# Kernel optimization log

Hardware: AMD Instinct MI355X
Metric: run time of the kernel (lower is better)

Reference implementation:

```python
import jax, jax.numpy as jnp
import numpy as np

OBJ_DIM, REL_DIM, EFF_DIM = 5, 1, 100
REL_HID, OBJ_HID, OUT_DIM = 150, 100, 2


def _init_linear(key, fan_in, fan_out):
    kw, kb = jax.random.split(key)
    bound = 1.0 / np.sqrt(fan_in)
    W = jax.random.uniform(kw, (fan_in, fan_out), jnp.float32, -bound, bound)
    b = jax.random.uniform(kb, (fan_out,), jnp.float32, -bound, bound)
    return W, b


def setup_inputs() -> dict:
    key = jax.random.key(0)
    ks = jax.random.split(key, 12)
    B, N, R = 64, 100, 9900
    inp = {
        "objects": jax.random.normal(ks[0], (B, N, OBJ_DIM), jnp.float32),
        "sender_relations": jax.random.uniform(ks[1], (B, N, R), jnp.float32),
        "receiver_relations": jax.random.uniform(ks[2], (B, N, R), jnp.float32),
        "relation_info": jax.random.normal(ks[3], (B, R, REL_DIM), jnp.float32),
    }
    # relational MLP: (2*obj + rel) -> 150 -> 150 -> effect_dim, ReLU after each
    rW1, rb1 = _init_linear(ks[4], 2 * OBJ_DIM + REL_DIM, REL_HID)
    rW2, rb2 = _init_linear(ks[5], REL_HID, REL_HID)
    rW3, rb3 = _init_linear(ks[6], REL_HID, EFF_DIM)
    # object MLP: (obj + effect) -> 100 -> 100 -> 2
    oW1, ob1 = _init_linear(ks[7], OBJ_DIM + EFF_DIM, OBJ_HID)
    oW2, ob2 = _init_linear(ks[8], OBJ_HID, OBJ_HID)
    oW3, ob3 = _init_linear(ks[9], OBJ_HID, OUT_DIM)
    inp.update(rW1=rW1, rb1=rb1, rW2=rW2, rb2=rb2, rW3=rW3, rb3=rb3,
               oW1=oW1, ob1=ob1, oW2=oW2, ob2=ob2, oW3=oW3, ob3=ob3)
    return inp


def _relational_mlp(x, rW1, rb1, rW2, rb2, rW3, rb3):
    h = jax.nn.relu(x @ rW1 + rb1)
    h = jax.nn.relu(h @ rW2 + rb2)
    return jax.nn.relu(h @ rW3 + rb3)


def _object_mlp(x, oW1, ob1, oW2, ob2, oW3, ob3):
    h = jax.nn.relu(x @ oW1 + ob1)
    h = jax.nn.relu(h @ oW2 + ob2)
    return h @ oW3 + ob3


def reference(objects, sender_relations, receiver_relations, relation_info,
              rW1, rb1, rW2, rb2, rW3, rb3, oW1, ob1, oW2, ob2, oW3, ob3):
    # gather: [B,R,N] @ [B,N,D] -> [B,R,D]
    senders = jnp.einsum('bnr,bnd->brd', sender_relations, objects)
    receivers = jnp.einsum('bnr,bnd->brd', receiver_relations, objects)
    rel_in = jnp.concatenate([senders, receivers, relation_info], axis=2)
    effects = _relational_mlp(rel_in, rW1, rb1, rW2, rb2, rW3, rb3)  # [B,R,E]
    # scatter: [B,N,R] @ [B,R,E] -> [B,N,E]
    effect_receivers = jnp.einsum('bnr,bre->bne', receiver_relations, effects)
    obj_in = jnp.concatenate([objects, effect_receivers], axis=2)
    return _object_mlp(obj_in, oW1, ob1, oW2, ob2, oW3, ob3)  # [B,N,2]
```

## Files before the change

### kernel.cpp

```cpp
#include <hip/hip_runtime.h>
#include <hip/hip_bf16.h>

#define B_    64
#define N_    100
#define R_    9900
#define OBJD  5
#define EFF   100

typedef __bf16 bf16x8 __attribute__((ext_vector_type(8)));
typedef __bf16 bf16x2 __attribute__((ext_vector_type(2)));
typedef short  short8v __attribute__((ext_vector_type(8)));
typedef float  f32x4  __attribute__((ext_vector_type(4)));

__device__ __forceinline__ ushort f2bf(float f) {
    __bf16 h = (__bf16)f;
    return __builtin_bit_cast(ushort, h);
}
__device__ __forceinline__ unsigned pk2(float a, float b) {
    bf16x2 v; v[0] = (__bf16)a; v[1] = (__bf16)b;
    return __builtin_bit_cast(unsigned, v);
}
__device__ __forceinline__ float bf2f(ushort u) {
    union { unsigned u; float f; } x; x.u = ((unsigned)u) << 16;
    return x.f;
}

#define WTR_OBJ 52096

__global__ __launch_bounds__(256) void k_prepw(
    const float* __restrict__ W1, const float* __restrict__ W2,
    const float* __restrict__ W3, const float* __restrict__ O1,
    const float* __restrict__ O2, const float* __restrict__ O3,
    ushort* __restrict__ WTR)
{
    const int img = blockIdx.x;
    if (img == 0) {
        for (int idx = threadIdx.x; idx < 6400; idx += 256) {
            const int c = idx / 40, k = idx - (idx/40)*40;
            WTR[idx] = f2bf((c < 150 && k < 11) ? W1[k*150 + c] : 0.f);
        }
    } else if (img == 1) {
        for (int idx = threadIdx.x; idx < 26880; idx += 256) {
            const int c = idx / 168, k = idx - (idx/168)*168;
            WTR[6400 + idx] = f2bf((c < 150 && k < 150) ? W2[k*150 + c] : 0.f);
        }
    } else if (img == 2) {
        for (int idx = threadIdx.x; idx < 18816; idx += 256) {
            const int c = idx / 168, k = idx - (idx/168)*168;
            WTR[33280 + idx] = f2bf((c < 100 && k < 150) ? W3[k*100 + c] : 0.f);
        }
    } else {
        const int j = img - 3;
        ushort* dst = WTR + WTR_OBJ + (size_t)j*11520;
        for (int idx = threadIdx.x; idx < 11520; idx += 256) {
            const int cc = idx / 72, kk = idx - (idx/72)*72;
            float v = 0.f;
            if (kk < 64) {
                if (j < 4) {
                    const int kg = j*64 + kk;
                    int row = -1;
                    if (kg < 5) row = kg;
                    else if (kg >= 8 && kg < 108) row = kg - 3;
                    else if (kg >= 108 && kg < 208) row = kg - 103;
                    if (cc < 100 && row >= 0) v = O1[row*100 + cc];
                } else if (j < 6) {
                    const int kg = (j-4)*64 + kk;
                    if (cc < 100 && kg < 100) v = O2[kg*100 + cc];
                } else {
                    const int kg = (j-6)*64 + kk;
                    if (cc < 2 && kg < 100) v = O3[kg*2 + cc];
                }
            }
            dst[idx] = f2bf(v);
        }
    }
}

#define LW1 0
#define LW2 6400
#define LW3 33280
#define LBA 52096
#define LBB 60160
#define LACT 68224
#define LBIAS 78976
#define LGB  79776
#define LTOT 81312

__global__ __launch_bounds__(512, 1) void k_relmlp_p(
    const float* __restrict__ obj, const float* __restrict__ SR,
    const float* __restrict__ RR, const float* __restrict__ RI,
    const ushort* __restrict__ WTR,
    const float* __restrict__ b1, const float* __restrict__ b2,
    const float* __restrict__ b3, float* __restrict__ ER)
{
    __shared__ __align__(16) ushort lds[LTOT];
    const int t  = threadIdx.x;
    const int b  = blockIdx.x >> 2;
    const int qt = blockIdx.x & 3;
    const int lane = t & 63, w = t >> 6;
    const int lo = lane & 15, hi = lane >> 4;
    const int mt = w & 3, nh = w >> 2;
    const int q  = t & 7,  rr = t >> 3;

    #pragma unroll
    for (int j = 0; j < 13; ++j) {
        const int idx = t + j*512;
        if (idx < 6512)
            reinterpret_cast<uint4*>(lds)[idx] =
                reinterpret_cast<const uint4*>(WTR)[idx];
    }
    {
        float* bias_w = (float*)(lds + LBIAS);
        if (t < 150)      bias_w[t] = b1[t];
        else if (t < 300) bias_w[t] = b2[t-150];
        else if (t < 400) bias_w[t] = b3[t-300];
    }
    if (t < 216) {
        ushort* base = lds + ((t < 108) ? LBA : LBB) + 100*72;
        const int k = (t < 108) ? t : t - 108;
        *reinterpret_cast<uint4*>(base + k*8) = make_uint4(0u, 0u, 0u, 0u);
    }
    if (t < 64) {
        ushort* gb0 = lds + LGB + t*24;
        gb0[11] = 0;
        *reinterpret_cast<ushort4*>(&gb0[12]) = make_ushort4(0,0,0,0);
        *reinterpret_cast<ushort4*>(&gb0[16]) = make_ushort4(0,0,0,0);
        *reinterpret_cast<ushort4*>(&gb0[20]) = make_ushort4(0,0,0,0);
    }

    float objv[13][5];
    {
        const int n0 = q*13;
        #pragma unroll
        for (int i = 0; i < 13; ++i) {
            const int n = n0 + i;
            #pragma unroll
            for (int d = 0; d < 5; ++d)
                objv[i][d] = (n < N_) ? obj[(size_t)b*500 + n*5 + d] : 0.f;
        }
    }

    const int tile0 = qt*39;
    const int tile1 = (tile0 + 39 < 155) ? tile0 + 39 : 155;

    ushort* bufA = lds + LBA;
    ushort* bufB = lds + LBB;
    ushort* act  = lds + LACT;
    ushort* gb   = lds + LGB;
    const float* bias = (const float*)(lds + LBIAS);

    f32x4 acc_er[7];
    #pragma unroll
    for (int ct = 0; ct < 7; ++ct) acc_er[ct] = (f32x4){0.f, 0.f, 0.f, 0.f};

    float4 psr[4], prr[4];
    float pri = 0.f, pri_n = 0.f;
    auto load4 = [&](float4* p, const float* M, int tile) {
        const int rr0 = tile*64;
        const int nr = (R_ - rr0 < 64) ? R_ - rr0 : 64;
        #pragma unroll
        for (int i = 0; i < 4; ++i) {
            const int idx = t + i*512;
            const int ci = idx < 1600 ? idx : 1599;
            const int n = ci >> 4, qq = ci & 15;
            const int col = (qq*4 < nr) ? qq*4 : 0;
            p[i] = *reinterpret_cast<const float4*>(
                &M[((size_t)b*N_ + n)*R_ + rr0 + col]);
        }
    };
    auto store4 = [&](const float4* p, ushort* dst, int nrow) {
        #pragma unroll
        for (int i = 0; i < 4; ++i) {
            const int idx = t + i*512;
            if (idx < 1600) {
                const int n = idx >> 4, qq = idx & 15;
                float4 v = p[i];
                if (qq*4 >= nrow) v = make_float4(0.f, 0.f, 0.f, 0.f);
                uint2 u; u.x = pk2(v.x, v.y); u.y = pk2(v.z, v.w);
                *reinterpret_cast<uint2*>(&dst[n*72 + qq*4]) = u;
            }
        }
    };
    auto loadRI = [&](int tile) -> float {
        const int rr0 = tile*64;
        return (t < 64 && rr0 + t < R_) ? RI[(size_t)b*R_ + rr0 + t] : 0.f;
    };

    load4(psr, SR, tile0);
    load4(prr, RR, tile0);
    pri = loadRI(tile0);
    __syncthreads();

    for (int tile = tile0; tile < tile1; ++tile) {
        const int r0 = tile*64;
        const int nrow = (R_ - r0 < 64) ? R_ - r0 : 64;

        store4(psr, bufA, nrow);
        store4(prr, bufB, nrow);
        if (tile + 1 < tile1) {
            load4(psr, SR, tile+1);
            load4(prr, RR, tile+1);
            pri_n = loadRI(tile+1);
        }
        __syncthreads();

        {
            float s0=0.f,s1=0.f,s2=0.f,s3=0.f,s4=0.f;
            float g0=0.f,g1=0.f,g2=0.f,g3=0.f,g4=0.f;
            const int n0 = q*13;
            #pragma unroll
            for (int i = 0; i < 13; ++i) {
                const int n = n0 + i;
                const float ms = bf2f(bufA[n*72 + rr]);
                const float mr = bf2f(bufB[n*72 + rr]);
                s0 += ms*objv[i][0]; s1 += ms*objv[i][1]; s2 += ms*objv[i][2];
                s3 += ms*objv[i][3]; s4 += ms*objv[i][4];
                g0 += mr*objv[i][0]; g1 += mr*objv[i][1]; g2 += mr*objv[i][2];
                g3 += mr*objv[i][3]; g4 += mr*objv[i][4];
            }
            #pragma unroll
            for (int msk = 1; msk < 8; msk <<= 1) {
                s0 += __shfl_xor(s0, msk); s1 += __shfl_xor(s1, msk);
                s2 += __shfl_xor(s2, msk); s3 += __shfl_xor(s3, msk);
                s4 += __shfl_xor(s4, msk);
                g0 += __shfl_xor(g0, msk); g1 += __shfl_xor(g1, msk);
                g2 += __shfl_xor(g2, msk); g3 += __shfl_xor(g3, msk);
                g4 += __shfl_xor(g4, msk);
            }
            if (q < 5) {
                const float sv = (q==0)?s0:(q==1)?s1:(q==2)?s2:(q==3)?s3:s4;
                const float gv = (q==0)?g0:(q==1)?g1:(q==2)?g2:(q==3)?g3:g4;
                gb[rr*24 + q]     = f2bf(sv);
                gb[rr*24 + 5 + q] = f2bf(gv);
            }
            if (t < 64) gb[t*24 + 10] = f2bf(pri);
            pri = pri_n;
        }
        __syncthreads();

        {
            f32x4 acc[5];
            #pragma unroll
            for (int j = 0; j < 5; ++j) {
                const int c = (nh*5 + j)*16 + lo;
                const float bv = (c < 150) ? bias[c] : 0.f;
                acc[j][0]=bv; acc[j][1]=bv; acc[j][2]=bv; acc[j][3]=bv;
            }
            bf16x8 a = __builtin_bit_cast(bf16x8, (short8v)0);
            if (hi < 2)
                a = *reinterpret_cast<const bf16x8*>(
                    &gb[(mt*16 + lo)*24 + hi*8]);
            #pragma unroll
            for (int j = 0; j < 5; ++j) {
                const int ct = nh*5 + j;
                const bf16x8 bb = *reinterpret_cast<const bf16x8*>(
                    &lds[LW1 + (ct*16 + lo)*40 + hi*8]);
                acc[j] = __builtin_amdgcn_mfma_f32_16x16x32_bf16(a, bb, acc[j], 0,0,0);
            }
            #pragma unroll
            for (int j = 0; j < 5; ++j) {
                const int ct = nh*5 + j;
                #pragma unroll
                for (int r = 0; r < 4; ++r)
                    act[(mt*16 + hi*4 + r)*168 + ct*16 + lo] =
                        f2bf(fmaxf(acc[j][r], 0.f));
            }
            __syncthreads();
        }
        {
            f32x4 acc[5];
            #pragma unroll
            for (int j = 0; j < 5; ++j) {
                const int c = (nh*5 + j)*16 + lo;
                const float bv = (c < 150) ? bias[150 + c] : 0.f;
                acc[j][0]=bv; acc[j][1]=bv; acc[j][2]=bv; acc[j][3]=bv;
            }
            #pragma unroll
            for (int ks = 0; ks < 5; ++ks) {
                const bf16x8 a = *reinterpret_cast<const bf16x8*>(
                    &act[(mt*16 + lo)*168 + ks*32 + hi*8]);
                #pragma unroll
                for (int j = 0; j < 5; ++j) {
                    const int ct = nh*5 + j;
                    const bf16x8 bb = *reinterpret_cast<const bf16x8*>(
                        &lds[LW2 + (ct*16 + lo)*168 + ks*32 + hi*8]);
                    acc[j] = __builtin_amdgcn_mfma_f32_16x16x32_bf16(a, bb, acc[j], 0,0,0);
                }
            }
            __syncthreads();
            #pragma unroll
            for (int j = 0; j < 5; ++j) {
                const int ct = nh*5 + j;
                #pragma unroll
                for (int r = 0; r < 4; ++r)
                    act[(mt*16 + hi*4 + r)*168 + ct*16 + lo] =
                        f2bf(fmaxf(acc[j][r], 0.f));
            }
            __syncthreads();
        }
        {
            const int nct = nh ? 3 : 4;
            f32x4 acc[4];
            #pragma unroll
            for (int j = 0; j < 4; ++j) {
                const int c = (nh*4 + j)*16 + lo;
                const float bv = (c < 100) ? bias[300 + c] : 0.f;
                acc[j][0]=bv; acc[j][1]=bv; acc[j][2]=bv; acc[j][3]=bv;
            }
            #pragma unroll
            for (int ks = 0; ks < 5; ++ks) {
                const bf16x8 a = *reinterpret_cast<const bf16x8*>(
                    &act[(mt*16 + lo)*168 + ks*32 + hi*8]);
                #pragma unroll
                for (int j = 0; j < 4; ++j) {
                    if (j < nct) {
                        const int ct = nh*4 + j;
                        const bf16x8 bb = *reinterpret_cast<const bf16x8*>(
                            &lds[LW3 + (ct*16 + lo)*168 + ks*32 + hi*8]);
                        acc[j] = __builtin_amdgcn_mfma_f32_16x16x32_bf16(a, bb, acc[j], 0,0,0);
                    }
                }
            }
            #pragma unroll
            for (int j = 0; j < 4; ++j) {
                if (j < nct) {
                    const int e = (nh*4 + j)*16 + lo;
                    if (e < 100) {
                        uint2 u;
                        u.x = pk2(fmaxf(acc[j][0], 0.f), fmaxf(acc[j][1], 0.f));
                        u.y = pk2(fmaxf(acc[j][2], 0.f), fmaxf(acc[j][3], 0.f));
                        *reinterpret_cast<uint2*>(&bufA[e*72 + mt*16 + hi*4]) = u;
                    }
                }
            }
            __syncthreads();
        }

        if (w < 7) {
            #pragma unroll
            for (int ks = 0; ks < 2; ++ks) {
                const bf16x8 a = *reinterpret_cast<const bf16x8*>(
                    &bufB[(w*16 + lo)*72 + ks*32 + hi*8]);
                #pragma unroll
                for (int ct = 0; ct < 7; ++ct) {
                    const bf16x8 bb = *reinterpret_cast<const bf16x8*>(
                        &bufA[(ct*16 + lo)*72 + ks*32 + hi*8]);
                    acc_er[ct] = __builtin_amdgcn_mfma_f32_16x16x32_bf16(
                        a, bb, acc_er[ct], 0, 0, 0);
                }
            }
        }
        __syncthreads();
    }

    if (w < 7) {
        float* ERq = ER + ((size_t)qt*B_ + b)*(size_t)(N_*EFF);
        #pragma unroll
        for (int ct = 0; ct < 7; ++ct) {
            const int e = ct*16 + lo;
            if (e < EFF) {
                #pragma unroll
                for (int rg = 0; rg < 4; ++rg) {
                    const int n = w*16 + hi*4 + rg;
                    if (n < N_)
                        ERq[n*EFF + e] = acc_er[ct][rg];
                }
            }
        }
    }
}

__device__ __forceinline__ void img_load(const ushort* __restrict__ g,
                                         uint4* pre, int t) {
    #pragma unroll
    for (int j = 0; j < 6; ++j) {
        int idx = t + j*256;
        int cidx = idx < 1440 ? idx : 1439;
        pre[j] = *reinterpret_cast<const uint4*>(g + (size_t)cidx*8);
    }
}
__device__ __forceinline__ void img_store(const uint4* pre, ushort* wt, int t) {
    #pragma unroll
    for (int j = 0; j < 6; ++j) {
        int idx = t + j*256;
        if (idx < 1440)
            *reinterpret_cast<uint4*>(wt + (size_t)idx*8) = pre[j];
    }
}

template<int COUT, int NCHUNK, int LASTKS, int NCT, bool RELU, int EPI, int ASTR>
__device__ __forceinline__ void mfma_layerO(
    const ushort* __restrict__ WT, const float* __restrict__ Bias,
    ushort* act, ushort* wt, int t, float* gout, int grow0)
{
    const int lane = t & 63;
    const int wv   = t >> 6;
    const int lo   = lane & 15;
    const int hi   = lane >> 4;

    f32x4 acc[2][NCT];
    #pragma unroll
    for (int ct = 0; ct < NCT; ++ct) {
        const int c = ct*16 + lo;
        const float bv = (c < COUT) ? Bias[c] : 0.f;
        #pragma unroll
        for (int m = 0; m < 2; ++m) {
            acc[m][ct][0] = bv; acc[m][ct][1] = bv;
            acc[m][ct][2] = bv; acc[m][ct][3] = bv;
        }
    }

    uint4 pre[6];
    img_load(WT, pre, t);
    #pragma unroll
    for (int q = 0; q < NCHUNK; ++q) {
        __syncthreads();
        img_store(pre, wt, t);
        if (q + 1 < NCHUNK) img_load(WT + (size_t)(q+1)*11520, pre, t);
        __syncthreads();
        const int nks = (q == NCHUNK-1) ? LASTKS : 2;
        #pragma unroll
        for (int ks = 0; ks < 2; ++ks) {
            if (ks < nks) {
                const int kg = q*64 + ks*32;
                const bf16x8 a0 = *reinterpret_cast<const bf16x8*>(
                    &act[(wv*32 +      lo)*ASTR + kg + hi*8]);
                const bf16x8 a1 = *reinterpret_cast<const bf16x8*>(
                    &act[(wv*32 + 16 + lo)*ASTR + kg + hi*8]);
                #pragma unroll
                for (int ct = 0; ct < NCT; ++ct) {
                    const bf16x8 b = *reinterpret_cast<const bf16x8*>(
                        &wt[(ct*16 + lo)*72 + ks*32 + hi*8]);
                    acc[0][ct] = __builtin_amdgcn_mfma_f32_16x16x32_bf16(
                        a0, b, acc[0][ct], 0, 0, 0);
                    acc[1][ct] = __builtin_amdgcn_mfma_f32_16x16x32_bf16(
                        a1, b, acc[1][ct], 0, 0, 0);
                }
            }
        }
    }

    __syncthreads();
    if (EPI == 0) {
        #pragma unroll
        for (int m = 0; m < 2; ++m)
            #pragma unroll
            for (int ct = 0; ct < NCT; ++ct)
                #pragma unroll
                for (int r = 0; r < 4; ++r) {
                    float v = acc[m][ct][r];
                    if (RELU) v = fmaxf(v, 0.f);
                    act[(wv*32 + m*16 + hi*4 + r)*ASTR + ct*16 + lo] = f2bf(v);
                }
    } else {
        #pragma unroll
        for (int m = 0; m < 2; ++m)
            #pragma unroll
            for (int r = 0; r < 4; ++r)
                if (lo < 2)
                    gout[(size_t)(grow0 + wv*32 + m*16 + hi*4 + r)*2 + lo] =
                        acc[m][0][r];
    }
    __syncthreads();
}

#define OSTR 232
#define ERSL ((size_t)B_*N_*EFF)

__global__ __launch_bounds__(256, 1) void k_objmlp_mfma(
    const float* __restrict__ obj, const float* __restrict__ ER,
    const ushort* __restrict__ WO,
    const float* __restrict__ ob1, const float* __restrict__ ob2,
    const float* __restrict__ ob3, float* __restrict__ out)
{
    __shared__ __align__(16) ushort act[128*OSTR];
    __shared__ __align__(16) ushort wt[160*72];
    const int t = threadIdx.x;
    const int rowbase = blockIdx.x * 128;

    float4 per[13];
    #pragma unroll
    for (int j = 0; j < 13; ++j) {
        const int idx = t + j*256;
        const int ci = idx < 3200 ? idx : 3199;
        const int row = ci / 25, c = ci - row*25;
        const float* p = &ER[(size_t)(rowbase + row)*100 + c*4];
        const float4 a0 = *reinterpret_cast<const float4*>(p);
        const float4 a1 = *reinterpret_cast<const float4*>(p + ERSL);
        const float4 a2 = *reinterpret_cast<const float4*>(p + 2*ERSL);
        const float4 a3 = *reinterpret_cast<const float4*>(p + 3*ERSL);
        per[j] = make_float4(a0.x + a1.x + a2.x + a3.x,
                             a0.y + a1.y + a2.y + a3.y,
                             a0.z + a1.z + a2.z + a3.z,
                             a0.w + a1.w + a2.w + a3.w);
    }
    #pragma unroll
    for (int j = 0; j < 13; ++j) {
        const int idx = t + j*256;
        if (idx < 3200) {
            const int row = idx / 25, c = idx - row*25;
            ushort h[4], l[4];
            #pragma unroll
            for (int k = 0; k < 4; ++k) {
                const float f = ((const float*)&per[j])[k];
                h[k] = f2bf(f);
                l[k] = f2bf(f - bf2f(h[k]));
            }
            *reinterpret_cast<ushort4*>(&act[row*OSTR + 8 + c*4]) =
                make_ushort4(h[0], h[1], h[2], h[3]);
            *reinterpret_cast<ushort4*>(&act[row*OSTR + 108 + c*4]) =
                make_ushort4(l[0], l[1], l[2], l[3]);
        }
    }
    #pragma unroll
    for (int j = 0; j < 3; ++j) {
        const int idx = t + j*256;
        if (idx < 640) {
            const int row = idx / 5, d = idx - row*5;
            act[row*OSTR + d] = f2bf(obj[(size_t)(rowbase + row)*5 + d]);
        }
    }
    #pragma unroll
    for (int j = 0; j < 2; ++j) {
        const int idx = t + j*256;
        if (idx < 384) {
            const int row = idx / 3, c = 5 + (idx - row*3);
            act[row*OSTR + c] = 0;
        }
    }
    #pragma unroll
    for (int j = 0; j < 2; ++j) {
        const int idx = t + j*256;
        if (idx < 512) {
            const int row = idx >> 2, p = idx & 3;
            *reinterpret_cast<ushort4*>(&act[row*OSTR + 208 + p*4]) =
                make_ushort4(0, 0, 0, 0);
        }
    }

    mfma_layerO<100, 4, 1, 7, true,  0, OSTR>(WO,           ob1, act, wt, t, nullptr, 0);
    mfma_layerO<100, 2, 2, 7, true,  0, OSTR>(WO + 4*11520, ob2, act, wt, t, nullptr, 0);
    mfma_layerO<2,   2, 2, 1, false, 2, OSTR>(WO + 6*11520, ob3, act, wt, t, out, rowbase);
}

extern "C" void kernel_launch(void* const* d_in, const int* in_sizes, int n_in,
                              void* d_out, int out_size, void* d_ws, size_t ws_size,
                              hipStream_t stream)
{
    const float* objects = (const float*)d_in[0];
    const float* SR      = (const float*)d_in[1];
    const float* RR      = (const float*)d_in[2];
    const float* RI      = (const float*)d_in[3];
    const float* rW1 = (const float*)d_in[4];  const float* rb1 = (const float*)d_in[5];
    const float* rW2 = (const float*)d_in[6];  const float* rb2 = (const float*)d_in[7];
    const float* rW3 = (const float*)d_in[8];  const float* rb3 = (const float*)d_in[9];
    const float* oW1 = (const float*)d_in[10]; const float* ob1 = (const float*)d_in[11];
    const float* oW2 = (const float*)d_in[12]; const float* ob2 = (const float*)d_in[13];
    const float* oW3 = (const float*)d_in[14]; const float* ob3 = (const float*)d_in[15];
    float* out = (float*)d_out;

    char* ws = (char*)d_ws;
    float*  ERp = (float*)ws;
    ushort* WTR = (ushort*)(ws + (size_t)4*B_*N_*EFF*sizeof(float));

    k_prepw<<<dim3(11), 256, 0, stream>>>(rW1, rW2, rW3, oW1, oW2, oW3, WTR);

    k_relmlp_p<<<dim3(256), 512, 0, stream>>>(objects, SR, RR, RI, WTR,
                                              rb1, rb2, rb3, ERp);

    k_objmlp_mfma<<<dim3(50), 256, 0, stream>>>(objects, ERp, WTR + WTR_OBJ,
                                                ob1, ob2, ob3, out);
}
```

Before: 366.9 us.

## Stage relation tiles via async global-to-LDS loads and hold W2 in registers

Replaces the register-prefetch-then-store staging of the sender/receiver relation tiles with direct global_load_lds transfers into fp32 LDS buffers. The next tile's transfer is issued after the gather phase so it overlaps the MLP compute. The layer-2 weight fragments are moved from LDS into registers, which frees LDS space, and launch bounds now ask for 2 blocks per CU. The costs are higher register pressure from the 25 bf16x8 weight fragments, an extra bf16 conversion pass for the receiver matrix, and possible register spills under the new occupancy target.

```diff
diff --git a/kernel.cpp b/kernel.cpp
--- a/kernel.cpp
+++ b/kernel.cpp
@@ -9,7 +9,6 @@
 
 typedef __bf16 bf16x8 __attribute__((ext_vector_type(8)));
 typedef __bf16 bf16x2 __attribute__((ext_vector_type(2)));
-typedef short  short8v __attribute__((ext_vector_type(8)));
 typedef float  f32x4  __attribute__((ext_vector_type(4)));
 
 __device__ __forceinline__ ushort f2bf(float f) {
@@ -23,6 +22,10 @@
 __device__ __forceinline__ float bf2f(ushort u) {
     union { unsigned u; float f; } x; x.u = ((unsigned)u) << 16;
     return x.f;
+}
+
+__device__ __forceinline__ void gload_lds16(const float* g, float* l) {
+    __builtin_amdgcn_global_load_lds((const void*)g, (void*)l, 16, 0, 0);
 }
 
 #define WTR_OBJ 52096
@@ -76,17 +79,18 @@
     }
 }
 
-#define LW1 0
-#define LW2 6400
-#define LW3 33280
-#define LBA 52096
-#define LBB 60160
-#define LACT 68224
-#define LBIAS 78976
-#define LGB  79776
-#define LTOT 81312
-
-__global__ __launch_bounds__(512, 1) void k_relmlp_p(
+#define LW1   0
+#define LW3   6400
+#define LSR32 25216
+#define LRR32 38528
+#define LRRNR 51840
+#define LEBUF 59904
+#define LACT  67968
+#define LBIAS 78720
+#define LGB   79520
+#define LTOT  81056
+
+__global__ __launch_bounds__(512, 2) void k_relmlp_p(
     const float* __restrict__ obj, const float* __restrict__ SR,
     const float* __restrict__ RR, const float* __restrict__ RI,
     const ushort* __restrict__ WTR,
@@ -102,12 +106,27 @@
     const int mt = w & 3, nh = w >> 2;
     const int q  = t & 7,  rr = t >> 3;
 
-    #pragma unroll
-    for (int j = 0; j < 13; ++j) {
+    float*  SRf  = (float*)(lds + LSR32);
+    float*  RRf  = (float*)(lds + LRR32);
+    ushort* RRnr = lds + LRRNR;
+    ushort* EB   = lds + LEBUF;
+    ushort* act  = lds + LACT;
+    ushort* gb   = lds + LGB;
+    const float* bias = (const float*)(lds + LBIAS);
+
+    #pragma unroll
+    for (int j = 0; j < 2; ++j) {
         const int idx = t + j*512;
-        if (idx < 6512)
+        if (idx < 800)
             reinterpret_cast<uint4*>(lds)[idx] =
                 reinterpret_cast<const uint4*>(WTR)[idx];
+    }
+    #pragma unroll
+    for (int j = 0; j < 5; ++j) {
+        const int idx = t + j*512;
+        if (idx < 2352)
+            reinterpret_cast<uint4*>(lds + LW3)[idx] =
+                reinterpret_cast<const uint4*>(WTR + 33280)[idx];
     }
     {
         float* bias_w = (float*)(lds + LBIAS);
@@ -115,13 +134,17 @@
         else if (t < 300) bias_w[t] = b2[t-150];
         else if (t < 400) bias_w[t] = b3[t-300];
     }
+    if (t < 256) {
+        SRf[6400 + t] = 0.f;
+        RRf[6400 + t] = 0.f;
+    }
     if (t < 216) {
-        ushort* base = lds + ((t < 108) ? LBA : LBB) + 100*72;
+        ushort* base = ((t < 108) ? RRnr : EB) + 100*72;
         const int k = (t < 108) ? t : t - 108;
         *reinterpret_cast<uint4*>(base + k*8) = make_uint4(0u, 0u, 0u, 0u);
     }
     if (t < 64) {
-        ushort* gb0 = lds + LGB + t*24;
+        ushort* gb0 = gb + t*24;
         gb0[11] = 0;
         *reinterpret_cast<ushort4*>(&gb0[12]) = make_ushort4(0,0,0,0);
         *reinterpret_cast<ushort4*>(&gb0[16]) = make_ushort4(0,0,0,0);
@@ -140,44 +163,35 @@
         }
     }
 
+    bf16x8 w2f[5][5];
+    #pragma unroll
+    for (int ks = 0; ks < 5; ++ks)
+        #pragma unroll
+        for (int j = 0; j < 5; ++j)
+            w2f[ks][j] = *reinterpret_cast<const bf16x8*>(
+                &WTR[6400 + ((nh*5 + j)*16 + lo)*168 + ks*32 + hi*8]);
+
     const int tile0 = qt*39;
     const int tile1 = (tile0 + 39 < 155) ? tile0 + 39 : 155;
 
-    ushort* bufA = lds + LBA;
-    ushort* bufB = lds + LBB;
-    ushort* act  = lds + LACT;
-    ushort* gb   = lds + LGB;
-    const float* bias = (const float*)(lds + LBIAS);
-
     f32x4 acc_er[7];
     #pragma unroll
     for (int ct = 0; ct < 7; ++ct) acc_er[ct] = (f32x4){0.f, 0.f, 0.f, 0.f};
 
-    float4 psr[4], prr[4];
-    float pri = 0.f, pri_n = 0.f;
-    auto load4 = [&](float4* p, const float* M, int tile) {
-        const int rr0 = tile*64;
-        const int nr = (R_ - rr0 < 64) ? R_ - rr0 : 64;
-        #pragma unroll
-        for (int i = 0; i < 4; ++i) {
-            const int idx = t + i*512;
-            const int ci = idx < 1600 ? idx : 1599;
-            const int n = ci >> 4, qq = ci & 15;
-            const int col = (qq*4 < nr) ? qq*4 : 0;
-            p[i] = *reinterpret_cast<const float4*>(
-                &M[((size_t)b*N_ + n)*R_ + rr0 + col]);
-        }
-    };
-    auto store4 = [&](const float4* p, ushort* dst, int nrow) {
-        #pragma unroll
-        for (int i = 0; i < 4; ++i) {
-            const int idx = t + i*512;
-            if (idx < 1600) {
-                const int n = idx >> 4, qq = idx & 15;
-                float4 v = p[i];
-                if (qq*4 >= nrow) v = make_float4(0.f, 0.f, 0.f, 0.f);
-                uint2 u; u.x = pk2(v.x, v.y); u.y = pk2(v.z, v.w);
-                *reinterpret_cast<uint2*>(&dst[n*72 + qq*4]) = u;
+    auto stage_async = [&](int tile) {
+        const int r0n = tile*64;
+        const int cb  = (lane & 15)*4;
+        const int cc  = (r0n + cb + 3 < R_) ? cb : 0;
+        const int rw  = lane >> 4;
+        const float* gS = SR + (size_t)b*N_*R_ + r0n + cc;
+        const float* gR = RR + (size_t)b*N_*R_ + r0n + cc;
+        #pragma unroll
+        for (int g0 = 0; g0 < 4; ++g0) {
+            const int g = w + g0*8;
+            if (g < 25) {
+                const int n = g*4;
+                gload_lds16(gS + (size_t)(n + rw)*R_, &SRf[n*64]);
+                gload_lds16(gR + (size_t)(n + rw)*R_, &RRf[n*64]);
             }
         }
     };
@@ -186,23 +200,15 @@
         return (t < 64 && rr0 + t < R_) ? RI[(size_t)b*R_ + rr0 + t] : 0.f;
     };
 
-    load4(psr, SR, tile0);
-    load4(prr, RR, tile0);
+    float pri, pri_n = 0.f;
+    stage_async(tile0);
     pri = loadRI(tile0);
+    asm volatile("s_waitcnt vmcnt(0)" ::: "memory");
     __syncthreads();
 
     for (int tile = tile0; tile < tile1; ++tile) {
         const int r0 = tile*64;
         const int nrow = (R_ - r0 < 64) ? R_ - r0 : 64;
-
-        store4(psr, bufA, nrow);
-        store4(prr, bufB, nrow);
-        if (tile + 1 < tile1) {
-            load4(psr, SR, tile+1);
-            load4(prr, RR, tile+1);
-            pri_n = loadRI(tile+1);
-        }
-        __syncthreads();
 
         {
             float s0=0.f,s1=0.f,s2=0.f,s3=0.f,s4=0.f;
@@ -211,8 +217,8 @@
             #pragma unroll
             for (int i = 0; i < 13; ++i) {
                 const int n = n0 + i;
-                const float ms = bf2f(bufA[n*72 + rr]);
-                const float mr = bf2f(bufB[n*72 + rr]);
+                const float ms = SRf[n*64 + rr];
+                const float mr = RRf[n*64 + rr];
                 s0 += ms*objv[i][0]; s1 += ms*objv[i][1]; s2 += ms*objv[i][2];
                 s3 += ms*objv[i][3]; s4 += ms*objv[i][4];
                 g0 += mr*objv[i][0]; g1 += mr*objv[i][1]; g2 += mr*objv[i][2];
@@ -234,9 +240,29 @@
                 gb[rr*24 + 5 + q] = f2bf(gv);
             }
             if (t < 64) gb[t*24 + 10] = f2bf(pri);
-            pri = pri_n;
+        }
+        {
+            #pragma unroll
+            for (int i = 0; i < 4; ++i) {
+                const int idx = t + i*512;
+                if (idx < 1600) {
+                    const int n = idx >> 4, qq = idx & 15;
+                    f32x4 v = *reinterpret_cast<const f32x4*>(&RRf[n*64 + qq*4]);
+                    if (qq*4 + 0 >= nrow) v[0] = 0.f;
+                    if (qq*4 + 1 >= nrow) v[1] = 0.f;
+                    if (qq*4 + 2 >= nrow) v[2] = 0.f;
+                    if (qq*4 + 3 >= nrow) v[3] = 0.f;
+                    uint2 u; u.x = pk2(v[0], v[1]); u.y = pk2(v[2], v[3]);
+                    *reinterpret_cast<uint2*>(&RRnr[n*72 + qq*4]) = u;
+                }
+            }
         }
         __syncthreads();
+
+        if (tile + 1 < tile1) {
+            stage_async(tile + 1);
+            pri_n = loadRI(tile + 1);
+        }
 
         {
             f32x4 acc[5];
@@ -246,7 +272,7 @@
                 const float bv = (c < 150) ? bias[c] : 0.f;
                 acc[j][0]=bv; acc[j][1]=bv; acc[j][2]=bv; acc[j][3]=bv;
             }
-            bf16x8 a = __builtin_bit_cast(bf16x8, (short8v)0);
+            bf16x8 a = {};
             if (hi < 2)
                 a = *reinterpret_cast<const bf16x8*>(
                     &gb[(mt*16 + lo)*24 + hi*8]);
@@ -280,12 +306,9 @@
                 const bf16x8 a = *reinterpret_cast<const bf16x8*>(
                     &act[(mt*16 + lo)*168 + ks*32 + hi*8]);
                 #pragma unroll
-                for (int j = 0; j < 5; ++j) {
-                    const int ct = nh*5 + j;
-                    const bf16x8 bb = *reinterpret_cast<const bf16x8*>(
-                        &lds[LW2 + (ct*16 + lo)*168 + ks*32 + hi*8]);
-                    acc[j] = __builtin_amdgcn_mfma_f32_16x16x32_bf16(a, bb, acc[j], 0,0,0);
-                }
+                for (int j = 0; j < 5; ++j)
+                    acc[j] = __builtin_amdgcn_mfma_f32_16x16x32_bf16(
+                        a, w2f[ks][j], acc[j], 0,0,0);
             }
             __syncthreads();
             #pragma unroll
@@ -329,7 +352,7 @@
                         uint2 u;
                         u.x = pk2(fmaxf(acc[j][0], 0.f), fmaxf(acc[j][1], 0.f));
                         u.y = pk2(fmaxf(acc[j][2], 0.f), fmaxf(acc[j][3], 0.f));
-                        *reinterpret_cast<uint2*>(&bufA[e*72 + mt*16 + hi*4]) = u;
+                        *reinterpret_cast<uint2*>(&EB[e*72 + mt*16 + hi*4]) = u;
                     }
                 }
             }
@@ -340,17 +363,19 @@
             #pragma unroll
             for (int ks = 0; ks < 2; ++ks) {
                 const bf16x8 a = *reinterpret_cast<const bf16x8*>(
-                    &bufB[(w*16 + lo)*72 + ks*32 + hi*8]);
+                    &RRnr[(w*16 + lo)*72 + ks*32 + hi*8]);
                 #pragma unroll
                 for (int ct = 0; ct < 7; ++ct) {
                     const bf16x8 bb = *reinterpret_cast<const bf16x8*>(
-                        &bufA[(ct*16 + lo)*72 + ks*32 + hi*8]);
+                        &EB[(ct*16 + lo)*72 + ks*32 + hi*8]);
                     acc_er[ct] = __builtin_amdgcn_mfma_f32_16x16x32_bf16(
                         a, bb, acc_er[ct], 0, 0, 0);
                 }
             }
         }
+        asm volatile("s_waitcnt vmcnt(0)" ::: "memory");
         __syncthreads();
+        pri = pri_n;
     }
 
     if (w < 7) {
```

New measurement: 627.8 us. +71.1%, slower.

## Hold part of W2 in registers to shrink LDS and fit two blocks per CU

Applied to the files above, without the earlier changes.

The first three k-slices of the layer-2 weight fragments move into per-thread registers, loaded once from global memory. Only the remaining two k-slices of W2 stay in LDS, in a compacted layout. The LDS footprint drops to about 132KB, and launch bounds change to allow two 512-thread blocks per CU, aiming to overlap memory streaming and MFMA work across blocks. The cost is 60 extra VGPRs per thread under a tighter register cap, which risks spills.

```diff
diff --git a/kernel.cpp b/kernel.cpp
--- a/kernel.cpp
+++ b/kernel.cpp
@@ -9,8 +9,8 @@
 
 typedef __bf16 bf16x8 __attribute__((ext_vector_type(8)));
 typedef __bf16 bf16x2 __attribute__((ext_vector_type(2)));
-typedef short  short8v __attribute__((ext_vector_type(8)));
 typedef float  f32x4  __attribute__((ext_vector_type(4)));
+typedef unsigned u32x4v __attribute__((ext_vector_type(4)));
 
 __device__ __forceinline__ ushort f2bf(float f) {
     __bf16 h = (__bf16)f;
@@ -76,17 +76,17 @@
     }
 }
 
-#define LW1 0
-#define LW2 6400
-#define LW3 33280
-#define LBA 52096
-#define LBB 60160
-#define LACT 68224
-#define LBIAS 78976
-#define LGB  79776
-#define LTOT 81312
-
-__global__ __launch_bounds__(512, 1) void k_relmlp_p(
+#define LW1   0
+#define LW3   6400
+#define LW2H  25216
+#define LBA   36736
+#define LBB   44800
+#define LACT  52864
+#define LBIAS 63616
+#define LGB   64416
+#define LTOT  65952
+
+__global__ __launch_bounds__(512, 2) void k_relmlp_p(
     const float* __restrict__ obj, const float* __restrict__ SR,
     const float* __restrict__ RR, const float* __restrict__ RI,
     const ushort* __restrict__ WTR,
@@ -102,12 +102,34 @@
     const int mt = w & 3, nh = w >> 2;
     const int q  = t & 7,  rr = t >> 3;
 
-    #pragma unroll
-    for (int j = 0; j < 13; ++j) {
+    ushort* bufA = lds + LBA;
+    ushort* bufB = lds + LBB;
+    ushort* act  = lds + LACT;
+    ushort* gb   = lds + LGB;
+    const float* bias = (const float*)(lds + LBIAS);
+
+    #pragma unroll
+    for (int j = 0; j < 2; ++j) {
         const int idx = t + j*512;
-        if (idx < 6512)
+        if (idx < 800)
             reinterpret_cast<uint4*>(lds)[idx] =
                 reinterpret_cast<const uint4*>(WTR)[idx];
+    }
+    #pragma unroll
+    for (int j = 0; j < 5; ++j) {
+        const int idx = t + j*512;
+        if (idx < 2352)
+            reinterpret_cast<uint4*>(lds + LW3)[idx] =
+                reinterpret_cast<const uint4*>(WTR + 33280)[idx];
+    }
+    #pragma unroll
+    for (int j = 0; j < 3; ++j) {
+        const int u = t + j*512;
+        if (u < 1280) {
+            const int c = u >> 3, p = u & 7;
+            *reinterpret_cast<uint4*>(lds + LW2H + c*72 + p*8) =
+                *reinterpret_cast<const uint4*>(WTR + 6400 + c*168 + 96 + p*8);
+        }
     }
     {
         float* bias_w = (float*)(lds + LBIAS);
@@ -116,12 +138,12 @@
         else if (t < 400) bias_w[t] = b3[t-300];
     }
     if (t < 216) {
-        ushort* base = lds + ((t < 108) ? LBA : LBB) + 100*72;
+        ushort* base = ((t < 108) ? bufA : bufB) + 100*72;
         const int k = (t < 108) ? t : t - 108;
         *reinterpret_cast<uint4*>(base + k*8) = make_uint4(0u, 0u, 0u, 0u);
     }
     if (t < 64) {
-        ushort* gb0 = lds + LGB + t*24;
+        ushort* gb0 = gb + t*24;
         gb0[11] = 0;
         *reinterpret_cast<ushort4*>(&gb0[12]) = make_ushort4(0,0,0,0);
         *reinterpret_cast<ushort4*>(&gb0[16]) = make_ushort4(0,0,0,0);
@@ -140,14 +162,19 @@
         }
     }
 
+    bf16x8 w2f[3][5];
+    #pragma unroll
+    for (int ks = 0; ks < 3; ++ks)
+        #pragma unroll
+        for (int j = 0; j < 5; ++j) {
+            u32x4v tmp = *reinterpret_cast<const u32x4v*>(
+                &WTR[6400 + ((nh*5 + j)*16 + lo)*168 + ks*32 + hi*8]);
+            asm volatile("" : "+v"(tmp));
+            w2f[ks][j] = __builtin_bit_cast(bf16x8, tmp);
+        }
+
     const int tile0 = qt*39;
     const int tile1 = (tile0 + 39 < 155) ? tile0 + 39 : 155;
-
-    ushort* bufA = lds + LBA;
-    ushort* bufB = lds + LBB;
-    ushort* act  = lds + LACT;
-    ushort* gb   = lds + LGB;
-    const float* bias = (const float*)(lds + LBIAS);
 
     f32x4 acc_er[7];
     #pragma unroll
@@ -246,7 +273,7 @@
                 const float bv = (c < 150) ? bias[c] : 0.f;
                 acc[j][0]=bv; acc[j][1]=bv; acc[j][2]=bv; acc[j][3]=bv;
             }
-            bf16x8 a = __builtin_bit_cast(bf16x8, (short8v)0);
+            bf16x8 a = {};
             if (hi < 2)
                 a = *reinterpret_cast<const bf16x8*>(
                     &gb[(mt*16 + lo)*24 + hi*8]);
@@ -276,15 +303,24 @@
                 acc[j][0]=bv; acc[j][1]=bv; acc[j][2]=bv; acc[j][3]=bv;
             }
             #pragma unroll
-            for (int ks = 0; ks < 5; ++ks) {
+            for (int ks = 0; ks < 3; ++ks) {
                 const bf16x8 a = *reinterpret_cast<const bf16x8*>(
                     &act[(mt*16 + lo)*168 + ks*32 + hi*8]);
                 #pragma unroll
+                for (int j = 0; j < 5; ++j)
+                    acc[j] = __builtin_amdgcn_mfma_f32_16x16x32_bf16(
+                        a, w2f[ks][j], acc[j], 0,0,0);
+            }
+            #pragma unroll
+            for (int ks = 3; ks < 5; ++ks) {
+                const bf16x8 a = *reinterpret_cast<const bf16x8*>(
+                    &act[(mt*16 + lo)*168 + ks*32 + hi*8]);
+                #pragma unroll
                 for (int j = 0; j < 5; ++j) {
-                    const int ct = nh*5 + j;
                     const bf16x8 bb = *reinterpret_cast<const bf16x8*>(
-                        &lds[LW2 + (ct*16 + lo)*168 + ks*32 + hi*8]);
-                    acc[j] = __builtin_amdgcn_mfma_f32_16x16x32_bf16(a, bb, acc[j], 0,0,0);
+                        &lds[LW2H + ((nh*5 + j)*16 + lo)*72 + (ks-3)*32 + hi*8]);
+                    acc[j] = __builtin_amdgcn_mfma_f32_16x16x32_bf16(
+                        a, bb, acc[j], 0,0,0);
                 }
             }
             __syncthreads();
```

Result: slower. 558.8 us (+52.3%).

## Stream W2/W3 from global in MFMA fragment layout, double-buffer relation tiles

Applied to the files above, without the earlier changes.

The W2 and W3 weights are pre-packed by two new prep blocks into a per-lane MFMA fragment layout and read directly from global/L2 instead of being staged in LDS. This frees LDS for double-buffered SR/RR tiles and separate activation buffers, and launch bounds allow two blocks per CU. The staging store for the next tile now overlaps with compute, which removes one barrier per tile. The cost is repeated global weight reads in every block and higher register pressure at two blocks per CU.

```diff
diff --git a/kernel.cpp b/kernel.cpp
--- a/kernel.cpp
+++ b/kernel.cpp
@@ -9,7 +9,6 @@
 
 typedef __bf16 bf16x8 __attribute__((ext_vector_type(8)));
 typedef __bf16 bf16x2 __attribute__((ext_vector_type(2)));
-typedef short  short8v __attribute__((ext_vector_type(8)));
 typedef float  f32x4  __attribute__((ext_vector_type(4)));
 
 __device__ __forceinline__ ushort f2bf(float f) {
@@ -26,6 +25,8 @@
 }
 
 #define WTR_OBJ 52096
+#define W2F_OFF 144256
+#define W3F_OFF 169856
 
 __global__ __launch_bounds__(256) void k_prepw(
     const float* __restrict__ W1, const float* __restrict__ W2,
@@ -48,6 +49,24 @@
         for (int idx = threadIdx.x; idx < 18816; idx += 256) {
             const int c = idx / 168, k = idx - (idx/168)*168;
             WTR[33280 + idx] = f2bf((c < 100 && k < 150) ? W3[k*100 + c] : 0.f);
+        }
+    } else if (img == 11) {
+        for (int idx = threadIdx.x; idx < 25600; idx += 256) {
+            const int ctks = idx >> 9;
+            const int ct = ctks / 5, ks = ctks - ct*5;
+            const int lane = (idx >> 3) & 63, e = idx & 7;
+            const int c = ct*16 + (lane & 15);
+            const int k = ks*32 + (lane >> 4)*8 + e;
+            WTR[W2F_OFF + idx] = f2bf((c < 150 && k < 150) ? W2[k*150 + c] : 0.f);
+        }
+    } else if (img == 12) {
+        for (int idx = threadIdx.x; idx < 17920; idx += 256) {
+            const int ctks = idx >> 9;
+            const int ct = ctks / 5, ks = ctks - ct*5;
+            const int lane = (idx >> 3) & 63, e = idx & 7;
+            const int c = ct*16 + (lane & 15);
+            const int k = ks*32 + (lane >> 4)*8 + e;
+            WTR[W3F_OFF + idx] = f2bf((c < 100 && k < 150) ? W3[k*100 + c] : 0.f);
         }
     } else {
         const int j = img - 3;
@@ -76,17 +95,18 @@
     }
 }
 
-#define LW1 0
-#define LW2 6400
-#define LW3 33280
-#define LBA 52096
-#define LBB 60160
-#define LACT 68224
-#define LBIAS 78976
-#define LGB  79776
-#define LTOT 81312
-
-__global__ __launch_bounds__(512, 1) void k_relmlp_p(
+#define LW1   0
+#define LBA0  6400
+#define LBB0  14464
+#define LBA1  22528
+#define LBB1  30592
+#define LACT0 38656
+#define LACT1 49408
+#define LBIAS 60160
+#define LGB   60960
+#define LTOT  62496
+
+__global__ __launch_bounds__(512, 2) void k_relmlp_p(
     const float* __restrict__ obj, const float* __restrict__ SR,
     const float* __restrict__ RR, const float* __restrict__ RI,
     const ushort* __restrict__ WTR,
@@ -102,10 +122,15 @@
     const int mt = w & 3, nh = w >> 2;
     const int q  = t & 7,  rr = t >> 3;
 
-    #pragma unroll
-    for (int j = 0; j < 13; ++j) {
+    ushort* act0 = lds + LACT0;
+    ushort* act1 = lds + LACT1;
+    ushort* gb   = lds + LGB;
+    const float* bias = (const float*)(lds + LBIAS);
+
+    #pragma unroll
+    for (int j = 0; j < 2; ++j) {
         const int idx = t + j*512;
-        if (idx < 6512)
+        if (idx < 800)
             reinterpret_cast<uint4*>(lds)[idx] =
                 reinterpret_cast<const uint4*>(WTR)[idx];
     }
@@ -115,13 +140,14 @@
         else if (t < 300) bias_w[t] = b2[t-150];
         else if (t < 400) bias_w[t] = b3[t-300];
     }
-    if (t < 216) {
-        ushort* base = lds + ((t < 108) ? LBA : LBB) + 100*72;
-        const int k = (t < 108) ? t : t - 108;
+    if (t < 432) {
+        const int bsel = t / 108;
+        const int k = t - bsel*108;
+        ushort* base = lds + LBA0 + bsel*8064 + 100*72;
         *reinterpret_cast<uint4*>(base + k*8) = make_uint4(0u, 0u, 0u, 0u);
     }
     if (t < 64) {
-        ushort* gb0 = lds + LGB + t*24;
+        ushort* gb0 = gb + t*24;
         gb0[11] = 0;
         *reinterpret_cast<ushort4*>(&gb0[12]) = make_ushort4(0,0,0,0);
         *reinterpret_cast<ushort4*>(&gb0[16]) = make_ushort4(0,0,0,0);
@@ -142,12 +168,6 @@
 
     const int tile0 = qt*39;
     const int tile1 = (tile0 + 39 < 155) ? tile0 + 39 : 155;
-
-    ushort* bufA = lds + LBA;
-    ushort* bufB = lds + LBB;
-    ushort* act  = lds + LACT;
-    ushort* gb   = lds + LGB;
-    const float* bias = (const float*)(lds + LBIAS);
 
     f32x4 acc_er[7];
     #pragma unroll
@@ -186,23 +206,37 @@
         return (t < 64 && rr0 + t < R_) ? RI[(size_t)b*R_ + rr0 + t] : 0.f;
     };
 
-    load4(psr, SR, tile0);
-    load4(prr, RR, tile0);
-    pri = loadRI(tile0);
+    {
+        const int nr0 = (R_ - tile0*64 < 64) ? R_ - tile0*64 : 64;
+        load4(psr, SR, tile0);
+        load4(prr, RR, tile0);
+        store4(psr, lds + LBA0, nr0);
+        store4(prr, lds + LBB0, nr0);
+        if (tile0 + 1 < tile1) {
+            load4(psr, SR, tile0 + 1);
+            load4(prr, RR, tile0 + 1);
+        }
+        pri = loadRI(tile0);
+    }
     __syncthreads();
 
+    int cur = 0;
     for (int tile = tile0; tile < tile1; ++tile) {
-        const int r0 = tile*64;
-        const int nrow = (R_ - r0 < 64) ? R_ - r0 : 64;
-
-        store4(psr, bufA, nrow);
-        store4(prr, bufB, nrow);
+        ushort* bAc = lds + LBA0 + cur*16128;
+        ushort* bBc = bAc + 8064;
+        ushort* bAn = lds + LBA0 + (cur^1)*16128;
+        ushort* bBn = bAn + 8064;
+
         if (tile + 1 < tile1) {
-            load4(psr, SR, tile+1);
-            load4(prr, RR, tile+1);
-            pri_n = loadRI(tile+1);
-        }
-        __syncthreads();
+            const int nr1 = (R_ - (tile+1)*64 < 64) ? R_ - (tile+1)*64 : 64;
+            store4(psr, bAn, nr1);
+            store4(prr, bBn, nr1);
+            if (tile + 2 < tile1) {
+                load4(psr, SR, tile + 2);
+                load4(prr, RR, tile + 2);
+            }
+            pri_n = loadRI(tile + 1);
+        }
 
         {
             float s0=0.f,s1=0.f,s2=0.f,s3=0.f,s4=0.f;
@@ -211,8 +245,8 @@
             #pragma unroll
             for (int i = 0; i < 13; ++i) {
                 const int n = n0 + i;
-                const float ms = bf2f(bufA[n*72 + rr]);
-                const float mr = bf2f(bufB[n*72 + rr]);
+                const float ms = bf2f(bAc[n*72 + rr]);
+                const float mr = bf2f(bBc[n*72 + rr]);
                 s0 += ms*objv[i][0]; s1 += ms*objv[i][1]; s2 += ms*objv[i][2];
                 s3 += ms*objv[i][3]; s4 += ms*objv[i][4];
                 g0 += mr*objv[i][0]; g1 += mr*objv[i][1]; g2 += mr*objv[i][2];
@@ -246,7 +280,7 @@
                 const float bv = (c < 150) ? bias[c] : 0.f;
                 acc[j][0]=bv; acc[j][1]=bv; acc[j][2]=bv; acc[j][3]=bv;
             }
-            bf16x8 a = __builtin_bit_cast(bf16x8, (short8v)0);
+            bf16x8 a = {};
             if (hi < 2)
                 a = *reinterpret_cast<const bf16x8*>(
                     &gb[(mt*16 + lo)*24 + hi*8]);
@@ -262,12 +296,14 @@
                 const int ct = nh*5 + j;
                 #pragma unroll
                 for (int r = 0; r < 4; ++r)
-                    act[(mt*16 + hi*4 + r)*168 + ct*16 + lo] =
+                    act0[(mt*16 + hi*4 + r)*168 + ct*16 + lo] =
                         f2bf(fmaxf(acc[j][r], 0.f));
             }
             __syncthreads();
         }
         {
+            const ushort* w2p = WTR + W2F_OFF + (size_t)lane*8 + (size_t)nh*12800;
+            asm volatile("" : "+v"(w2p));
             f32x4 acc[5];
             #pragma unroll
             for (int j = 0; j < 5; ++j) {
@@ -278,27 +314,31 @@
             #pragma unroll
             for (int ks = 0; ks < 5; ++ks) {
                 const bf16x8 a = *reinterpret_cast<const bf16x8*>(
-                    &act[(mt*16 + lo)*168 + ks*32 + hi*8]);
-                #pragma unroll
-                for (int j = 0; j < 5; ++j) {
-                    const int ct = nh*5 + j;
-                    const bf16x8 bb = *reinterpret_cast<const bf16x8*>(
-                        &lds[LW2 + (ct*16 + lo)*168 + ks*32 + hi*8]);
-                    acc[j] = __builtin_amdgcn_mfma_f32_16x16x32_bf16(a, bb, acc[j], 0,0,0);
-                }
-            }
-            __syncthreads();
+                    &act0[(mt*16 + lo)*168 + ks*32 + hi*8]);
+                const bf16x8 b0 = *reinterpret_cast<const bf16x8*>(w2p + ((0*5 + ks) << 9));
+                const bf16x8 b1v = *reinterpret_cast<const bf16x8*>(w2p + ((1*5 + ks) << 9));
+                const bf16x8 b2v = *reinterpret_cast<const bf16x8*>(w2p + ((2*5 + ks) << 9));
+                const bf16x8 b3v = *reinterpret_cast<const bf16x8*>(w2p + ((3*5 + ks) << 9));
+                const bf16x8 b4v = *reinterpret_cast<const bf16x8*>(w2p + ((4*5 + ks) << 9));
+                acc[0] = __builtin_amdgcn_mfma_f32_16x16x32_bf16(a, b0,  acc[0], 0,0,0);
+                acc[1] = __builtin_amdgcn_mfma_f32_16x16x32_bf16(a, b1v, acc[1], 0,0,0);
+                acc[2] = __builtin_amdgcn_mfma_f32_16x16x32_bf16(a, b2v, acc[2], 0,0,0);
+                acc[3] = __builtin_amdgcn_mfma_f32_16x16x32_bf16(a, b3v, acc[3], 0,0,0);
+                acc[4] = __builtin_amdgcn_mfma_f32_16x16x32_bf16(a, b4v, acc[4], 0,0,0);
+            }
             #pragma unroll
             for (int j = 0; j < 5; ++j) {
                 const int ct = nh*5 + j;
                 #pragma unroll
                 for (int r = 0; r < 4; ++r)
-                    act[(mt*16 + hi*4 + r)*168 + ct*16 + lo] =
+                    act1[(mt*16 + hi*4 + r)*168 + ct*16 + lo] =
                         f2bf(fmaxf(acc[j][r], 0.f));
             }
             __syncthreads();
         }
         {
+            const ushort* w3p = WTR + W3F_OFF + (size_t)lane*8 + (size_t)nh*10240;
+            asm volatile("" : "+v"(w3p));
             const int nct = nh ? 3 : 4;
             f32x4 acc[4];
             #pragma unroll
@@ -310,13 +350,12 @@
             #pragma unroll
             for (int ks = 0; ks < 5; ++ks) {
                 const bf16x8 a = *reinterpret_cast<const bf16x8*>(
-                    &act[(mt*16 + lo)*168 + ks*32 + hi*8]);
+                    &act1[(mt*16 + lo)*168 + ks*32 + hi*8]);
                 #pragma unroll
                 for (int j = 0; j < 4; ++j) {
                     if (j < nct) {
-                        const int ct = nh*4 + j;
                         const bf16x8 bb = *reinterpret_cast<const bf16x8*>(
-                            &lds[LW3 + (ct*16 + lo)*168 + ks*32 + hi*8]);
+                            w3p + ((j*5 + ks) << 9));
                         acc[j] = __builtin_amdgcn_mfma_f32_16x16x32_bf16(a, bb, acc[j], 0,0,0);
                     }
                 }
@@ -329,7 +368,7 @@
                         uint2 u;
                         u.x = pk2(fmaxf(acc[j][0], 0.f), fmaxf(acc[j][1], 0.f));
                         u.y = pk2(fmaxf(acc[j][2], 0.f), fmaxf(acc[j][3], 0.f));
-                        *reinterpret_cast<uint2*>(&bufA[e*72 + mt*16 + hi*4]) = u;
+                        *reinterpret_cast<uint2*>(&bAc[e*72 + mt*16 + hi*4]) = u;
                     }
                 }
             }
@@ -340,17 +379,18 @@
             #pragma unroll
             for (int ks = 0; ks < 2; ++ks) {
                 const bf16x8 a = *reinterpret_cast<const bf16x8*>(
-                    &bufB[(w*16 + lo)*72 + ks*32 + hi*8]);
+                    &bBc[(w*16 + lo)*72 + ks*32 + hi*8]);
                 #pragma unroll
                 for (int ct = 0; ct < 7; ++ct) {
                     const bf16x8 bb = *reinterpret_cast<const bf16x8*>(
-                        &bufA[(ct*16 + lo)*72 + ks*32 + hi*8]);
+                        &bAc[(ct*16 + lo)*72 + ks*32 + hi*8]);
                     acc_er[ct] = __builtin_amdgcn_mfma_f32_16x16x32_bf16(
                         a, bb, acc_er[ct], 0, 0, 0);
                 }
             }
         }
         __syncthreads();
+        cur ^= 1;
     }
 
     if (w < 7) {
@@ -563,7 +603,7 @@
     float*  ERp = (float*)ws;
     ushort* WTR = (ushort*)(ws + (size_t)4*B_*N_*EFF*sizeof(float));
 
-    k_prepw<<<dim3(11), 256, 0, stream>>>(rW1, rW2, rW3, oW1, oW2, oW3, WTR);
+    k_prepw<<<dim3(13), 256, 0, stream>>>(rW1, rW2, rW3, oW1, oW2, oW3, WTR);
 
     k_relmlp_p<<<dim3(256), 512, 0, stream>>>(objects, SR, RR, RI, WTR,
                                               rb1, rb2, rb3, ERp);
```

Measured after the change: 389.3 us. +6.1%, slower.
